# Performance work log

Measured on AMD Instinct MI355X. Metric: run time of the kernel, lower is better.

Reference implementation:

```python
import jax, jax.numpy as jnp
import numpy as np
import math

D_MODEL = 1024
N_HEADS = 16
D_HEAD = D_MODEL // N_HEADS


def setup_inputs() -> dict:
    key = jax.random.key(0)
    k_x, k_wqkv, k_bqkv, k_wp, k_bp = jax.random.split(key, 5)
    B, T = 2, 2048
    s = 1.0 / math.sqrt(D_MODEL)
    return {
        "x": jax.random.normal(k_x, (B, T, D_MODEL), dtype=jnp.float32),
        "W_qkv": jax.random.uniform(k_wqkv, (D_MODEL, 3 * D_MODEL), minval=-s, maxval=s, dtype=jnp.float32),
        "b_qkv": jax.random.uniform(k_bqkv, (3 * D_MODEL,), minval=-s, maxval=s, dtype=jnp.float32),
        "W_proj": jax.random.uniform(k_wp, (D_MODEL, D_MODEL), minval=-s, maxval=s, dtype=jnp.float32),
        "b_proj": jax.random.uniform(k_bp, (D_MODEL,), minval=-s, maxval=s, dtype=jnp.float32),
    }


def reference(x, W_qkv, b_qkv, W_proj, b_proj):
    B, T, C = x.shape
    qkv = x @ W_qkv + b_qkv                      # [B,T,3C]
    qkv = qkv.reshape(B, T, 3, N_HEADS, D_HEAD)
    qkv = jnp.transpose(qkv, (2, 0, 3, 1, 4))     # [3,B,H,T,dh]
    q, k, v = qkv[0], qkv[1], qkv[2]
    scale = math.sqrt(D_HEAD)
    attn = jnp.einsum('bhqd,bhkd->bhqk', q, k) / scale  # [B,H,T,T]
    causal = jnp.tril(jnp.ones((T, T), dtype=bool))
    attn = jnp.where(causal, attn, -jnp.inf)
    attn = jax.nn.softmax(attn, axis=-1)
    out = jnp.einsum('bhqk,bhkd->bhqd', attn, v)  # [B,H,T,dh]
    out = jnp.transpose(out, (0, 2, 1, 3)).reshape(B, T, C)
    return out @ W_proj + b_proj
```

## Files before the change

kernel.cpp:

```cpp
#include <hip/hip_runtime.h>

#define B_    2
#define T_    2048
#define C_    1024
#define H_    16
#define DH_   64
#define M_    (B_ * T_)
#define NQKV  (3 * C_)

typedef __bf16 bf16;
typedef __bf16 bf16x4 __attribute__((ext_vector_type(4)));
typedef __bf16 bf16x8 __attribute__((ext_vector_type(8)));
typedef float  f32x4  __attribute__((ext_vector_type(4)));

__device__ __forceinline__ void async16(const void* g, void* l) {
  __builtin_amdgcn_global_load_lds(
      (const __attribute__((address_space(1))) void*)g,
      (__attribute__((address_space(3))) void*)l, 16, 0, 0);
}

__global__ __launch_bounds__(256) void cvt_bf16_k(const float* __restrict__ in,
                                                  bf16* __restrict__ out) {
  const int i = (blockIdx.x * 256 + threadIdx.x) * 4;
  float4 v = *(const float4*)(in + i);
  bf16x4 o;
  o[0] = (bf16)v.x; o[1] = (bf16)v.y; o[2] = (bf16)v.z; o[3] = (bf16)v.w;
  *(bf16x4*)(out + i) = o;
}

__global__ __launch_bounds__(256) void transpose_cvt(const float* __restrict__ in,
                                                     bf16* __restrict__ out,
                                                     int R, int C) {
  __shared__ float tile[32][33];
  const int c0 = blockIdx.x * 32, r0 = blockIdx.y * 32;
  const int tx = threadIdx.x, ty = threadIdx.y;
#pragma unroll
  for (int j = 0; j < 4; j++)
    tile[ty + j * 8][tx] = in[(size_t)(r0 + ty + j * 8) * C + c0 + tx];
  __syncthreads();
#pragma unroll
  for (int j = 0; j < 4; j++)
    out[(size_t)(c0 + ty + j * 8) * R + r0 + tx] = (bf16)tile[tx][ty + j * 8];
}

template <int EPI, int BM>
__global__ __launch_bounds__(256) void gemm_k(
    const bf16* __restrict__ A, const bf16* __restrict__ Bt,
    const float* __restrict__ bias, float* __restrict__ outF,
    bf16* __restrict__ qb, bf16* __restrict__ kb, bf16* __restrict__ vtb) {
  constexpr int K = 1024;
  constexpr int MI = BM / 32;
  __shared__ alignas(16) bf16 As[BM * 64];
  __shared__ alignas(16) bf16 Bs[128 * 64];
  const int tid = threadIdx.x;
  const int lane = tid & 63, wv = tid >> 6;
  const int l15 = lane & 15, quad = lane >> 4;
  const int wm = (wv >> 1) * (BM / 2), wn = (wv & 1) * 64;
  const int m0 = blockIdx.x * BM, n0 = blockIdx.y * 128;

  f32x4 acc[MI][4] = {};

  const int srow = tid >> 3;
  const int sgb = ((tid & 7) ^ (srow & 7)) * 8;
  const bf16* ga = A + (size_t)(m0 + srow) * K + sgb;
  const bf16* gb = Bt + (size_t)(n0 + srow) * K + sgb;
  const int swz = l15 & 7;

  for (int it = 0; it < K / 64; ++it) {
    const int k0 = it * 64;
#pragma unroll
    for (int c = 0; c < BM / 32; c++)
      async16(ga + k0 + (size_t)(c * 32) * K, As + tid * 8 + c * 2048);
#pragma unroll
    for (int c = 0; c < 4; c++)
      async16(gb + k0 + (size_t)(c * 32) * K, Bs + tid * 8 + c * 2048);
    __syncthreads();
    bf16x8 af[2][MI], bfr[2][4];
#pragma unroll
    for (int kk = 0; kk < 2; kk++) {
#pragma unroll
      for (int i = 0; i < MI; i++)
        af[kk][i] = *(const bf16x8*)(As + (wm + i * 16 + l15) * 64 +
                                     (((kk * 4 + quad) ^ swz) << 3));
#pragma unroll
      for (int j = 0; j < 4; j++)
        bfr[kk][j] = *(const bf16x8*)(Bs + (wn + j * 16 + l15) * 64 +
                                      (((kk * 4 + quad) ^ swz) << 3));
    }
#pragma unroll
    for (int kk = 0; kk < 2; kk++)
#pragma unroll
      for (int i = 0; i < MI; i++)
#pragma unroll
        for (int j = 0; j < 4; j++)
          acc[i][j] = __builtin_amdgcn_mfma_f32_16x16x32_bf16(
              af[kk][i], bfr[kk][j], acc[i][j], 0, 0, 0);
    __syncthreads();
  }

#pragma unroll
  for (int i = 0; i < MI; i++) {
#pragma unroll
    for (int j = 0; j < 4; j++) {
      const int gcol = n0 + wn + j * 16 + l15;
      const float bv = bias[gcol];
      const int trow = m0 + wm + i * 16 + quad * 4;
      if constexpr (EPI == 0) {
        const int which = gcol >> 10;
        const int hn = gcol & 1023;
        const int h = hn >> 6, d = hn & 63;
        const int bb = trow >> 11, t = trow & 2047;
        const int head = bb * 16 + h;
        if (which == 0) {
#pragma unroll
          for (int r = 0; r < 4; r++)
            qb[head * 131072 + (t + r) * 64 + d] =
                (bf16)((acc[i][j][r] + bv) * 0.1803368801f);
        } else if (which == 1) {
#pragma unroll
          for (int r = 0; r < 4; r++)
            kb[head * 131072 + (t + r) * 64 + d] = (bf16)(acc[i][j][r] + bv);
        } else {
          bf16x4 pv;
#pragma unroll
          for (int r = 0; r < 4; r++) pv[r] = (bf16)(acc[i][j][r] + bv);
          *(bf16x4*)(vtb + head * 131072 + d * 2048 + t) = pv;
        }
      } else {
#pragma unroll
        for (int r = 0; r < 4; r++)
          outF[(size_t)(trow + r) * 1024 + gcol] = acc[i][j][r] + bv;
      }
    }
  }
}

__global__ __launch_bounds__(512, 4) void attn_k(const bf16* __restrict__ Q,
                                                 const bf16* __restrict__ K,
                                                 const bf16* __restrict__ Vt,
                                                 bf16* __restrict__ O) {
  __shared__ alignas(16) bf16 Ks[128 * 64];
  __shared__ alignas(16) bf16 Vs[2][64 * 128];
  __shared__ alignas(16) bf16 Ps[8][16 * 64];
  const int tid = threadIdx.x, lane = tid & 63, wv = tid >> 6;
  const int l15 = lane & 15, quad = lane >> 4;

  const int b = blockIdx.x;
  const int sH = b >> 8, i = b & 255;
  const int bh = (i & 7) | (((i >> 3) & 3) << 3);
  const int x = i >> 5;
  const int qJ = sH ? (15 - x) : x;
  const int q0 = qJ * 128;
  const int nIter = qJ + 1;

  const bf16* Qb = Q + (size_t)bh * 131072;
  const bf16* Kb = K + (size_t)bh * 131072;
  const bf16* Vb = Vt + (size_t)bh * 131072;

  const int krow = tid >> 3;
  const int kg = (tid & 7) ^ (krow & 7);
  const bf16* gk = Kb + krow * 64 + kg * 8;
  const int vrow = tid >> 4;
  const int vg = (tid & 15) ^ (vrow & 15);
  const bf16* gv = Vb + vrow * 2048 + vg * 8;

  const int swz7 = l15 & 7;
  bf16* Pw = Ps[wv];
  const int bb = bh >> 4, h = bh & 15;

  const int q = q0 + wv * 16 + l15;
  bf16x8 aq0 = *(const bf16x8*)(Qb + q * 64 + quad * 8);
  bf16x8 aq1 = *(const bf16x8*)(Qb + q * 64 + 32 + quad * 8);

  f32x4 o[4] = {};
  float m = -3.0e38f, lsum = 0.f;

  async16(gk, &Ks[tid * 8]);
  async16(gk + 64 * 64, &Ks[tid * 8 + 4096]);
  async16(gv, &Vs[0][tid * 8]);
  async16(gv + 32 * 2048, &Vs[0][tid * 8 + 4096]);

  for (int it = 0; it < nIter; ++it) {
    __syncthreads();
    const bf16* Vc = Vs[it & 1];

    bf16x8 kf0[8], kf1[8];
#pragma unroll
    for (int nf = 0; nf < 8; nf++)
      kf0[nf] = *(const bf16x8*)(Ks + (nf * 16 + l15) * 64 + ((quad ^ swz7) << 3));
#pragma unroll
    for (int nf = 0; nf < 8; nf++)
      kf1[nf] = *(const bf16x8*)(Ks + (nf * 16 + l15) * 64 + (((4 + quad) ^ swz7) << 3));

    f32x4 s[8] = {};
#pragma unroll
    for (int nf = 0; nf < 8; nf++)
      s[nf] = __builtin_amdgcn_mfma_f32_16x16x32_bf16(kf0[nf], aq0, s[nf], 0, 0, 0);

    __syncthreads();
    if (it + 1 < nIter) {
      const int kt1 = (it + 1) * 128;
      async16(gk + kt1 * 64, &Ks[tid * 8]);
      async16(gk + kt1 * 64 + 64 * 64, &Ks[tid * 8 + 4096]);
      async16(gv + kt1, &Vs[(it + 1) & 1][tid * 8]);
      async16(gv + kt1 + 32 * 2048, &Vs[(it + 1) & 1][tid * 8 + 4096]);
    }

#pragma unroll
    for (int nf = 0; nf < 8; nf++)
      s[nf] = __builtin_amdgcn_mfma_f32_16x16x32_bf16(kf1[nf], aq1, s[nf], 0, 0, 0);

    if (it == nIter - 1) {
#pragma unroll
      for (int nf = 0; nf < 8; nf++)
#pragma unroll
        for (int r = 0; r < 4; r++) {
          const int kt = it * 128 + nf * 16 + quad * 4 + r;
          if (kt > q) s[nf][r] = -3.0e38f;
        }
    }

    float mx = s[0][0];
#pragma unroll
    for (int nf = 0; nf < 8; nf++)
#pragma unroll
      for (int r = 0; r < 4; r++) mx = fmaxf(mx, s[nf][r]);
    mx = fmaxf(mx, __shfl_xor(mx, 16));
    mx = fmaxf(mx, __shfl_xor(mx, 32));
    const float mnew = fmaxf(m, mx);
    const float alpha = __builtin_amdgcn_exp2f(m - mnew);
    m = mnew;
    float ts = 0.f;
    bf16x4 p4[8];
#pragma unroll
    for (int nf = 0; nf < 8; nf++)
#pragma unroll
      for (int r = 0; r < 4; r++) {
        const float pv = __builtin_amdgcn_exp2f(s[nf][r] - mnew);
        ts += pv;
        p4[nf][r] = (bf16)pv;
      }
    ts += __shfl_xor(ts, 16);
    ts += __shfl_xor(ts, 32);
    lsum = lsum * alpha + ts;
#pragma unroll
    for (int nf = 0; nf < 4; nf++)
#pragma unroll
      for (int r = 0; r < 4; r++) o[nf][r] *= alpha;

#pragma unroll
    for (int half = 0; half < 2; half++) {
#pragma unroll
      for (int nf = 0; nf < 4; nf++)
        *(bf16x4*)(Pw + l15 * 64 + ((((nf << 1) | (quad >> 1)) ^ swz7) << 3) +
                   ((quad & 1) << 2)) = p4[half * 4 + nf];
      bf16x8 pb0 = *(const bf16x8*)(Pw + l15 * 64 + ((quad ^ swz7) << 3));
      bf16x8 pb1 = *(const bf16x8*)(Pw + l15 * 64 + (((4 + quad) ^ swz7) << 3));
#pragma unroll
      for (int kc = 0; kc < 2; kc++) {
        bf16x8 pb = kc ? pb1 : pb0;
        const int kcg = half * 2 + kc;
#pragma unroll
        for (int nf = 0; nf < 4; nf++) {
          bf16x8 vf = *(const bf16x8*)(Vc + (nf * 16 + l15) * 128 +
                                       (((kcg * 4 + quad) ^ l15) << 3));
          o[nf] = __builtin_amdgcn_mfma_f32_16x16x32_bf16(vf, pb, o[nf], 0, 0, 0);
        }
      }
    }
  }

  const float inv = 1.0f / lsum;
#pragma unroll
  for (int nf = 0; nf < 4; nf++) {
    bf16x4 ov;
#pragma unroll
    for (int r = 0; r < 4; r++) ov[r] = (bf16)(o[nf][r] * inv);
    *(bf16x4*)(O + (size_t)(bb * 2048 + q) * 1024 + h * 64 + nf * 16 + quad * 4) = ov;
  }
}

extern "C" void kernel_launch(void* const* d_in, const int* in_sizes, int n_in,
                              void* d_out, int out_size, void* d_ws, size_t ws_size,
                              hipStream_t stream) {
  const float* x     = (const float*)d_in[0];
  const float* Wqkv  = (const float*)d_in[1];
  const float* bqkv  = (const float*)d_in[2];
  const float* Wproj = (const float*)d_in[3];
  const float* bproj = (const float*)d_in[4];
  float* out = (float*)d_out;

  char* p = (char*)d_ws;
  bf16* xbf    = (bf16*)p; p += (size_t)M_ * C_ * 2;
  bf16* wqkvT  = (bf16*)p; p += (size_t)NQKV * C_ * 2;
  bf16* wprojT = (bf16*)p; p += (size_t)C_ * C_ * 2;
  bf16* Qb     = (bf16*)p; p += (size_t)M_ * C_ * 2;
  bf16* Kb     = (bf16*)p; p += (size_t)M_ * C_ * 2;
  bf16* Vtb    = (bf16*)p; p += (size_t)M_ * C_ * 2;
  bf16* AO     = (bf16*)p;

  cvt_bf16_k<<<M_ * C_ / 1024, 256, 0, stream>>>(x, xbf);
  transpose_cvt<<<dim3(NQKV / 32, C_ / 32), dim3(32, 8), 0, stream>>>(Wqkv, wqkvT, C_, NQKV);
  transpose_cvt<<<dim3(C_ / 32, C_ / 32), dim3(32, 8), 0, stream>>>(Wproj, wprojT, C_, C_);

  gemm_k<0, 64><<<dim3(M_ / 64, NQKV / 128), 256, 0, stream>>>(
      xbf, wqkvT, bqkv, nullptr, Qb, Kb, Vtb);

  attn_k<<<512, 512, 0, stream>>>(Qb, Kb, Vtb, AO);

  gemm_k<1, 64><<<dim3(M_ / 64, C_ / 128), 256, 0, stream>>>(
      AO, wprojT, bproj, out, nullptr, nullptr, nullptr);
}
```

Before: 169.9 us.

## Merge prep kernels, add MFMA priority hints, skip softmax rescale when max stable

Combines the x conversion and both weight transposes into one launch to cut launch overhead. Inside attention, it wraps MFMA blocks in s_setprio to favour matrix issue across waves. It also adds a lazy online-softmax rescale that skips the alpha multiply when the running max grows by at most 8 across the wave. This keeps numerics bounded, but exp2 values can reach up to 2^8 before bf16 conversion, which costs a little precision.

```diff
diff --git a/kernel.cpp b/kernel.cpp
--- a/kernel.cpp
+++ b/kernel.cpp
@@ -19,21 +19,30 @@
       (__attribute__((address_space(3))) void*)l, 16, 0, 0);
 }
 
-__global__ __launch_bounds__(256) void cvt_bf16_k(const float* __restrict__ in,
-                                                  bf16* __restrict__ out) {
-  const int i = (blockIdx.x * 256 + threadIdx.x) * 4;
-  float4 v = *(const float4*)(in + i);
-  bf16x4 o;
-  o[0] = (bf16)v.x; o[1] = (bf16)v.y; o[2] = (bf16)v.z; o[3] = (bf16)v.w;
-  *(bf16x4*)(out + i) = o;
-}
-
-__global__ __launch_bounds__(256) void transpose_cvt(const float* __restrict__ in,
-                                                     bf16* __restrict__ out,
-                                                     int R, int C) {
+__global__ __launch_bounds__(256) void prep_k(
+    const float* __restrict__ x, bf16* __restrict__ xbf,
+    const float* __restrict__ Wqkv, bf16* __restrict__ wqkvT,
+    const float* __restrict__ Wproj, bf16* __restrict__ wprojT) {
   __shared__ float tile[32][33];
-  const int c0 = blockIdx.x * 32, r0 = blockIdx.y * 32;
-  const int tx = threadIdx.x, ty = threadIdx.y;
+  const int bid = blockIdx.x;
+  if (bid < 4096) {
+    const int i = (bid * 256 + threadIdx.x) * 4;
+    float4 v = *(const float4*)(x + i);
+    bf16x4 o;
+    o[0] = (bf16)v.x; o[1] = (bf16)v.y; o[2] = (bf16)v.z; o[3] = (bf16)v.w;
+    *(bf16x4*)(xbf + i) = o;
+    return;
+  }
+  const float* in; bf16* out; int R, C, cb, rb;
+  if (bid < 4096 + 3072) {
+    const int b = bid - 4096;
+    in = Wqkv; out = wqkvT; R = 1024; C = 3072; cb = b % 96; rb = b / 96;
+  } else {
+    const int b = bid - 7168;
+    in = Wproj; out = wprojT; R = 1024; C = 1024; cb = b & 31; rb = b >> 5;
+  }
+  const int c0 = cb * 32, r0 = rb * 32;
+  const int tx = threadIdx.x & 31, ty = threadIdx.x >> 5;
 #pragma unroll
   for (int j = 0; j < 4; j++)
     tile[ty + j * 8][tx] = in[(size_t)(r0 + ty + j * 8) * C + c0 + tx];
@@ -193,9 +202,11 @@
       kf1[nf] = *(const bf16x8*)(Ks + (nf * 16 + l15) * 64 + (((4 + quad) ^ swz7) << 3));
 
     f32x4 s[8] = {};
+    __builtin_amdgcn_s_setprio(1);
 #pragma unroll
     for (int nf = 0; nf < 8; nf++)
       s[nf] = __builtin_amdgcn_mfma_f32_16x16x32_bf16(kf0[nf], aq0, s[nf], 0, 0, 0);
+    __builtin_amdgcn_s_setprio(0);
 
     __syncthreads();
     if (it + 1 < nIter) {
@@ -206,9 +217,11 @@
       async16(gv + kt1 + 32 * 2048, &Vs[(it + 1) & 1][tid * 8 + 4096]);
     }
 
+    __builtin_amdgcn_s_setprio(1);
 #pragma unroll
     for (int nf = 0; nf < 8; nf++)
       s[nf] = __builtin_amdgcn_mfma_f32_16x16x32_bf16(kf1[nf], aq1, s[nf], 0, 0, 0);
+    __builtin_amdgcn_s_setprio(0);
 
     if (it == nIter - 1) {
 #pragma unroll
@@ -227,26 +240,29 @@
       for (int r = 0; r < 4; r++) mx = fmaxf(mx, s[nf][r]);
     mx = fmaxf(mx, __shfl_xor(mx, 16));
     mx = fmaxf(mx, __shfl_xor(mx, 32));
-    const float mnew = fmaxf(m, mx);
-    const float alpha = __builtin_amdgcn_exp2f(m - mnew);
-    m = mnew;
+    if (!__all(mx - m <= 8.0f)) {
+      const float mnew = fmaxf(m, mx);
+      const float alpha = __builtin_amdgcn_exp2f(m - mnew);
+      m = mnew;
+      lsum *= alpha;
+#pragma unroll
+      for (int nf = 0; nf < 4; nf++)
+#pragma unroll
+        for (int r = 0; r < 4; r++) o[nf][r] *= alpha;
+    }
     float ts = 0.f;
     bf16x4 p4[8];
 #pragma unroll
     for (int nf = 0; nf < 8; nf++)
 #pragma unroll
       for (int r = 0; r < 4; r++) {
-        const float pv = __builtin_amdgcn_exp2f(s[nf][r] - mnew);
+        const float pv = __builtin_amdgcn_exp2f(s[nf][r] - m);
         ts += pv;
         p4[nf][r] = (bf16)pv;
       }
     ts += __shfl_xor(ts, 16);
     ts += __shfl_xor(ts, 32);
-    lsum = lsum * alpha + ts;
-#pragma unroll
-    for (int nf = 0; nf < 4; nf++)
-#pragma unroll
-      for (int r = 0; r < 4; r++) o[nf][r] *= alpha;
+    lsum += ts;
 
 #pragma unroll
     for (int half = 0; half < 2; half++) {
@@ -256,6 +272,7 @@
                    ((quad & 1) << 2)) = p4[half * 4 + nf];
       bf16x8 pb0 = *(const bf16x8*)(Pw + l15 * 64 + ((quad ^ swz7) << 3));
       bf16x8 pb1 = *(const bf16x8*)(Pw + l15 * 64 + (((4 + quad) ^ swz7) << 3));
+      __builtin_amdgcn_s_setprio(1);
 #pragma unroll
       for (int kc = 0; kc < 2; kc++) {
         bf16x8 pb = kc ? pb1 : pb0;
@@ -267,6 +284,7 @@
           o[nf] = __builtin_amdgcn_mfma_f32_16x16x32_bf16(vf, pb, o[nf], 0, 0, 0);
         }
       }
+      __builtin_amdgcn_s_setprio(0);
     }
   }
 
@@ -299,9 +317,7 @@
   bf16* Vtb    = (bf16*)p; p += (size_t)M_ * C_ * 2;
   bf16* AO     = (bf16*)p;
 
-  cvt_bf16_k<<<M_ * C_ / 1024, 256, 0, stream>>>(x, xbf);
-  transpose_cvt<<<dim3(NQKV / 32, C_ / 32), dim3(32, 8), 0, stream>>>(Wqkv, wqkvT, C_, NQKV);
-  transpose_cvt<<<dim3(C_ / 32, C_ / 32), dim3(32, 8), 0, stream>>>(Wproj, wprojT, C_, C_);
+  prep_k<<<8192, 256, 0, stream>>>(x, xbf, Wqkv, wqkvT, Wproj, wprojT);
 
   gemm_k<0, 64><<<dim3(M_ / 64, NQKV / 128), 256, 0, stream>>>(
       xbf, wqkvT, bqkv, nullptr, Qb, Kb, Vtb);
```

Result: no change. 173.1 us (+1.9%).
